# Kernel tuning notes

Measured on AMD Instinct MI355X. Metric: run time of the kernel, lower is better.

The kernel has to match this reference:

```python
import jax, jax.numpy as jnp
import numpy as np

D_MODEL = 1024
NUM_HEADS = 16
D_K = D_MODEL // NUM_HEADS
SCALE = 1.0 / np.sqrt(D_K).astype(np.float32)


def _rope_cos_sin(T, d_k):
    inv_freq = 1.0 / (10000.0 ** (jnp.arange(0, d_k, 2, dtype=jnp.float32) / d_k))
    t = jnp.arange(T, dtype=jnp.float32)
    freqs = jnp.outer(t, inv_freq)                      # [T, d_k/2]
    emb = jnp.concatenate([freqs, freqs], axis=-1)      # [T, d_k]
    return jnp.cos(emb)[None, None], jnp.sin(emb)[None, None]  # [1,1,T,d_k]


def _rotate_half(x):
    x1, x2 = x[..., : x.shape[-1] // 2], x[..., x.shape[-1] // 2 :]
    return jnp.concatenate([-x2, x1], axis=-1)


def setup_inputs() -> dict:
    key = jax.random.key(0)
    ks = jax.random.split(key, 8)
    B, T, C = 2, 2048, D_MODEL
    x = jax.random.normal(ks[0], (B, T, C), dtype=jnp.float32)
    # torch nn.Linear weights are [out, in]; forward does x @ W.T
    s = 1.0 / np.sqrt(C)
    Wq = jax.random.uniform(ks[1], (C, C), jnp.float32, -s, s)
    Wk = jax.random.uniform(ks[2], (C, C), jnp.float32, -s, s)
    Wv = jax.random.uniform(ks[3], (C, C), jnp.float32, -s, s)
    Wo = jax.random.uniform(ks[4], (C, C), jnp.float32, -s, s)
    bo = jax.random.uniform(ks[5], (C,), jnp.float32, -s, s)
    sector_bias = jnp.zeros((1, NUM_HEADS, 1, 1), dtype=jnp.float32)
    sector_weights = jax.random.uniform(ks[6], (B, T), jnp.float32, 0.5, 1.5)
    # causal mask, broadcastable to [B,H,T,T]; 0 -> masked
    mask = jnp.tril(jnp.ones((T, T), dtype=jnp.int32))[None, None]
    return {
        "x": x, "Wq": Wq, "Wk": Wk, "Wv": Wv, "Wo": Wo, "bo": bo,
        "sector_bias": sector_bias, "sector_weights": sector_weights,
        "mask": mask,
    }


def reference(x, Wq, Wk, Wv, Wo, bo, sector_bias, sector_weights, mask):
    B, T, C = x.shape
    H, dk = NUM_HEADS, D_K
    q = (x @ Wq.T).reshape(B, T, H, dk).transpose(0, 2, 1, 3)  # [B,H,T,dk]
    k = (x @ Wk.T).reshape(B, T, H, dk).transpose(0, 2, 1, 3)
    v = (x @ Wv.T).reshape(B, T, H, dk).transpose(0, 2, 1, 3)
    cos, sin = _rope_cos_sin(T, dk)
    q = q * cos + _rotate_half(q) * sin
    k = k * cos + _rotate_half(k) * sin
    scores = jnp.einsum("bhqd,bhkd->bhqk", q, k) * SCALE
    scores = scores + sector_bias
    scores = scores * sector_weights[:, None, None, :]  # broadcast over key dim
    scores = jnp.where(mask == 0, -jnp.inf, scores)
    attn = jax.nn.softmax(scores, axis=-1)
    out = jnp.einsum("bhqk,bhkd->bhqd", attn, v)
    out = out.transpose(0, 2, 1, 3).reshape(B, T, C)
    return out @ Wo.T + bo
```

## Files before the change

### kernel.cpp

```cpp
#include <hip/hip_runtime.h>


typedef __bf16 bf16x8 __attribute__((ext_vector_type(8)));
typedef float f32x4 __attribute__((ext_vector_type(4)));
typedef float f32x16 __attribute__((ext_vector_type(16)));
typedef unsigned short u16x8 __attribute__((ext_vector_type(8)));

__device__ __forceinline__ unsigned short f2bf(float f) {
    union { float f; unsigned int u; } c; c.f = f;
    unsigned int u = c.u;
    unsigned int r = u + 0x7fffu + ((u >> 16) & 1u);
    return (unsigned short)(r >> 16);
}
__device__ __forceinline__ unsigned cvtpk(float lo, float hi) {
    unsigned r;
    asm("v_cvt_pk_bf16_f32 %0, %1, %2" : "=v"(r) : "v"(lo), "v"(hi));
    return r;
}
__device__ __forceinline__ void plswap(unsigned a, unsigned b, unsigned& r0, unsigned& r1) {
#if __has_builtin(__builtin_amdgcn_permlane32_swap)
    auto s = __builtin_amdgcn_permlane32_swap(a, b, false, false);
    r0 = (unsigned)s[0]; r1 = (unsigned)s[1];
#else
    const int hh = (int)(threadIdx.x & 63) >> 5;
    const unsigned oa = (unsigned)__shfl_xor((int)a, 32);
    const unsigned ob = (unsigned)__shfl_xor((int)b, 32);
    r0 = hh ? ob : a;
    r1 = hh ? b : oa;
#endif
}
__device__ __forceinline__ void stage8_f32(unsigned short* dst, const float* src) {
    const float4 a = *(const float4*)src;
    const float4 b = *(const float4*)(src + 4);
    u16x8 v;
    v[0] = f2bf(a.x); v[1] = f2bf(a.y); v[2] = f2bf(a.z); v[3] = f2bf(a.w);
    v[4] = f2bf(b.x); v[5] = f2bf(b.y); v[6] = f2bf(b.z); v[7] = f2bf(b.w);
    *(u16x8*)dst = v;
}
__device__ __forceinline__ void async16(const unsigned short* g, unsigned short* l) {
    __builtin_amdgcn_global_load_lds(
        (const __attribute__((address_space(1))) void*)g,
        (__attribute__((address_space(3))) void*)l, 16, 0, 0);
}

__global__ __launch_bounds__(256) void cvt_all(
    const float* __restrict__ x, const float* __restrict__ Wq, const float* __restrict__ Wk,
    const float* __restrict__ Wv, const float* __restrict__ Wo,
    unsigned short* __restrict__ dst, int hasX, int n8)
{
    const int i = blockIdx.x * 256 + threadIdx.x;
    if (i >= n8) return;
    int r = i;
    const float* src; int off;
    const int xg = hasX ? 524288 : 0;
    if (r < xg) { src = x; off = r; }
    else {
        r -= xg;
        const int w = r >> 17, o = r & 131071;
        src = (w == 0) ? Wq : (w == 1) ? Wk : (w == 2) ? Wv : Wo;
        off = o;
    }
    stage8_f32(&dst[(size_t)i * 8], &src[(size_t)off * 8]);
}

template<int A_BF16>
__global__ __launch_bounds__(512) void gemm_qkv(
    const void* __restrict__ Av, const unsigned short* __restrict__ Wb,
    unsigned short* __restrict__ outv, const float* __restrict__ swg)
{
    constexpr int K = 1024, BK = 32, NS = K / BK;
    __shared__ __align__(16) unsigned short As[3][128 * BK];
    __shared__ __align__(16) unsigned short Bs[3][128 * BK];
    const int tid = threadIdx.x;
    const int wid = tid >> 6, lane = tid & 63, g = lane >> 4, l = lane & 15;
    const int wm = (wid & 3) * 32, wn = (wid >> 2) * 64;

    const int lin = blockIdx.x + (blockIdx.y << 3) + (blockIdx.z << 8);
    const int wg  = (lin & 7) * 96 + (lin >> 3);
    const int bx = wg & 7, by = (wg >> 3) & 31, bz = wg >> 8;
    const int m0 = by * 128, n0 = bx * 128;
    const int z = bz;
    const unsigned short* W = Wb + (size_t)z * 1048576;

    f32x4 acc[2][4];
#pragma unroll
    for (int i = 0; i < 2; ++i)
#pragma unroll
        for (int j = 0; j < 4; ++j) acc[i][j] = f32x4{0.f, 0.f, 0.f, 0.f};

    const int r  = tid >> 2;
    const int cs = (((tid & 3) ^ ((tid >> 3) & 3)) * 8);
    const int xg = (g ^ ((l >> 1) & 3)) * 8;

    auto compute = [&](int buf) {
        const unsigned short* Asr = As[buf];
        const unsigned short* Bsr = Bs[buf];
        bf16x8 af[2], bfr[4];
#pragma unroll
        for (int im = 0; im < 2; ++im) af[im]  = *(const bf16x8*)&Asr[(wm + im * 16 + l) * BK + xg];
#pragma unroll
        for (int in = 0; in < 4; ++in) bfr[in] = *(const bf16x8*)&Bsr[(wn + in * 16 + l) * BK + xg];
#pragma unroll
        for (int im = 0; im < 2; ++im)
#pragma unroll
            for (int in = 0; in < 4; ++in)
                acc[im][in] = __builtin_amdgcn_mfma_f32_16x16x32_bf16(af[im], bfr[in], acc[im][in], 0, 0, 0);
    };

    if (A_BF16) {
        const unsigned short* A = (const unsigned short*)Av;
        auto stage = [&](int buf, int k0) {
            async16(&A[(size_t)(m0 + r) * K + k0 + cs], &As[buf][wid * 512]);
            async16(&W[(size_t)(n0 + r) * K + k0 + cs], &Bs[buf][wid * 512]);
        };
        stage(0, 0);
        stage(1, BK);
        for (int ks = 0; ks < NS; ++ks) {
            if (ks + 1 < NS) asm volatile("s_waitcnt vmcnt(2)" ::: "memory");
            else             asm volatile("s_waitcnt vmcnt(0)" ::: "memory");
            __builtin_amdgcn_s_barrier();
            compute(ks % 3);
            if (ks + 2 < NS) stage((ks + 2) % 3, (ks + 2) * BK);
        }
    } else {
        auto stageF = [&](int buf, int k0) {
            const float* A = (const float*)Av;
            stage8_f32(&As[buf][r * BK + cs], &A[(size_t)(m0 + r) * K + k0 + cs]);
            async16(&W[(size_t)(n0 + r) * K + k0 + cs], &Bs[buf][wid * 512]);
        };
        stageF(0, 0);
        __syncthreads();
        for (int k0 = 0; k0 < K; k0 += BK) {
            const int cur = (k0 >> 5) & 1;
            if (k0 + BK < K) stageF(cur ^ 1, k0 + BK);
            compute(cur);
            __syncthreads();
        }
    }

    unsigned short* outq = outv + (size_t)z * 4194304;
    if (z < 2) {
        const int hq = (n0 + wn) >> 6;
        float freq[2];
#pragma unroll
        for (int in = 0; in < 2; ++in)
            freq[in] = exp2f(-(float)(in * 16 + l) * 0.41524101186f);
#pragma unroll
        for (int im = 0; im < 2; ++im)
#pragma unroll
            for (int i = 0; i < 4; ++i) {
                const int m = m0 + wm + im * 16 + g * 4 + i;
                const int b = m >> 11, t = m & 2047;
                float fw = 1.0f;
                if (z == 1) fw = 0.18033688011f * swg[(b << 11) + t];
                const size_t fq = (size_t)((b << 4) + hq) * 131072
                                + (size_t)((t >> 5) << 2) * 512
                                + (size_t)((((l >> 3) & 1) << 5) + (t & 31)) * 8 + (l & 7);
#pragma unroll
                for (int in = 0; in < 2; ++in) {
                    const float ang = (float)t * freq[in];
                    const float cs2 = __cosf(ang), sn = __sinf(ang);
                    const float x1 = acc[im][in][i], x2 = acc[im][in + 2][i];
                    outq[fq + (size_t)in * 512]       = f2bf((x1 * cs2 - x2 * sn) * fw);
                    outq[fq + (size_t)(in + 2) * 512] = f2bf((x2 * cs2 + x1 * sn) * fw);
                }
            }
    } else {
#pragma unroll
        for (int im = 0; im < 2; ++im)
#pragma unroll
            for (int in = 0; in < 4; ++in) {
                const int n = n0 + wn + in * 16 + l;
                const int h = n >> 6, d = n & 63;
                const int mb = m0 + wm + im * 16 + g * 4;
                const int bq = mb >> 11, t0 = mb & 2047;
                ushort4 pk;
                pk.x = f2bf(acc[im][in][0]); pk.y = f2bf(acc[im][in][1]);
                pk.z = f2bf(acc[im][in][2]); pk.w = f2bf(acc[im][in][3]);
                const size_t fv = (size_t)((bq << 4) + h) * 131072
                                + (size_t)(((t0 >> 5) << 2) + ((d >> 5) << 1) + ((t0 >> 4) & 1)) * 512
                                + (size_t)((((t0 >> 3) & 1) << 5) + (d & 31)) * 8 + (t0 & 7);
                *(ushort4*)&outq[fv] = pk;
            }
    }
}

__global__ __launch_bounds__(512) void gemm_proj(
    const unsigned short* __restrict__ A, const unsigned short* __restrict__ W,
    float* __restrict__ out, const float* __restrict__ bias)
{
    constexpr int K = 1024, BK = 32, NS = K / BK;
    __shared__ __align__(16) unsigned short As[3][64 * BK];
    __shared__ __align__(16) unsigned short Bs[3][128 * BK];
    const int tid = threadIdx.x;
    const int wid = tid >> 6, lane = tid & 63, g = lane >> 4, l = lane & 15;
    const int wm = (wid & 1) * 32, wn = (wid >> 1) * 32;

    const int lin = blockIdx.x + (blockIdx.y << 3);
    const int wg  = (lin & 7) * 64 + (lin >> 3);
    const int m0 = (wg >> 3) * 64, n0 = (wg & 7) * 128;

    f32x4 acc[2][2];
#pragma unroll
    for (int i = 0; i < 2; ++i)
#pragma unroll
        for (int j = 0; j < 2; ++j) acc[i][j] = f32x4{0.f, 0.f, 0.f, 0.f};

    const int r  = tid >> 2;
    const int cs = (((tid & 3) ^ ((tid >> 3) & 3)) * 8);
    const int xg = (g ^ ((l >> 1) & 3)) * 8;

    auto stage = [&](int buf, int k0) {
        if (tid < 256) async16(&A[(size_t)(m0 + r) * K + k0 + cs], &As[buf][wid * 512]);
        async16(&W[(size_t)(n0 + r) * K + k0 + cs], &Bs[buf][wid * 512]);
    };
    auto compute = [&](int buf) {
        const unsigned short* Asr = As[buf];
        const unsigned short* Bsr = Bs[buf];
        bf16x8 af[2], bfr[2];
#pragma unroll
        for (int im = 0; im < 2; ++im) af[im]  = *(const bf16x8*)&Asr[(wm + im * 16 + l) * BK + xg];
#pragma unroll
        for (int in = 0; in < 2; ++in) bfr[in] = *(const bf16x8*)&Bsr[(wn + in * 16 + l) * BK + xg];
#pragma unroll
        for (int im = 0; im < 2; ++im)
#pragma unroll
            for (int in = 0; in < 2; ++in)
                acc[im][in] = __builtin_amdgcn_mfma_f32_16x16x32_bf16(af[im], bfr[in], acc[im][in], 0, 0, 0);
    };

    stage(0, 0);
    stage(1, BK);
    for (int ks = 0; ks < NS; ++ks) {
        if (ks + 1 < NS) {
            if (wid < 4) asm volatile("s_waitcnt vmcnt(2)" ::: "memory");
            else         asm volatile("s_waitcnt vmcnt(1)" ::: "memory");
        } else {
            asm volatile("s_waitcnt vmcnt(0)" ::: "memory");
        }
        __builtin_amdgcn_s_barrier();
        compute(ks % 3);
        if (ks + 2 < NS) stage((ks + 2) % 3, (ks + 2) * BK);
    }

#pragma unroll
    for (int im = 0; im < 2; ++im)
#pragma unroll
        for (int in = 0; in < 2; ++in) {
            const int n = n0 + wn + in * 16 + l;
#pragma unroll
            for (int i = 0; i < 4; ++i) {
                const int m = m0 + wm + im * 16 + g * 4 + i;
                out[(size_t)m * 1024 + n] = acc[im][in][i] + bias[n];
            }
        }
}

__global__ __launch_bounds__(128, 2) void flash_attn(
    const unsigned short* __restrict__ Qf, const unsigned short* __restrict__ Kf,
    const unsigned short* __restrict__ Vf, const float* __restrict__ sbias,
    const float* __restrict__ sw, unsigned short* __restrict__ attn)
{
    constexpr int T = 2048;
    __shared__ float Cmb[3072];

    const int tid = threadIdx.x, wid = tid >> 6, lane = tid & 63;
    const int hl = lane & 31, hh = lane >> 5;
    const int id = blockIdx.x;
    const int p  = 63 - (id >> 5);
    const int bh = id & 31, b = bh >> 4, h = bh & 15;
    const size_t fb = (size_t)bh * 131072;
    const float bias = sbias[h];
    const float* swb = sw + b * T;

    bf16x8 onef;
#pragma unroll
    for (int j = 0; j < 8; ++j) onef[j] = (__bf16)1.0f;

    const int q0 = p * 32;
    bf16x8 qf[4];
#pragma unroll
    for (int ks = 0; ks < 4; ++ks)
        qf[ks] = *(const bf16x8*)&Qf[fb + (size_t)(p * 4 + ks) * 512 + lane * 8];

    f32x16 oacc[2], lrow;
#pragma unroll
    for (int r = 0; r < 16; ++r) { oacc[0][r] = 0.f; oacc[1][r] = 0.f; lrow[r] = 0.f; }

    bf16x8 kcur[4];
    if (wid <= p) {
        const unsigned short* kb = &Kf[fb + (size_t)wid * 2048 + lane * 8];
#pragma unroll
        for (int ks = 0; ks < 4; ++ks) kcur[ks] = *(const bf16x8*)&kb[ks * 512];
    }

    for (int c = wid; c <= p; c += 2) {
        f32x16 sx;
#pragma unroll
        for (int r = 0; r < 16; ++r) sx[r] = 0.f;
        sx = __builtin_amdgcn_mfma_f32_32x32x16_bf16(kcur[0], qf[0], sx, 0, 0, 0);
        sx = __builtin_amdgcn_mfma_f32_32x32x16_bf16(kcur[1], qf[1], sx, 0, 0, 0);
        sx = __builtin_amdgcn_mfma_f32_32x32x16_bf16(kcur[2], qf[2], sx, 0, 0, 0);
        sx = __builtin_amdgcn_mfma_f32_32x32x16_bf16(kcur[3], qf[3], sx, 0, 0, 0);

        if (c + 2 <= p) {
            const unsigned short* kb = &Kf[fb + (size_t)(c + 2) * 2048 + lane * 8];
#pragma unroll
            for (int ks = 0; ks < 4; ++ks) kcur[ks] = *(const bf16x8*)&kb[ks * 512];
        }

        const unsigned short* vb = &Vf[fb + (size_t)c * 2048 + lane * 8];
        const bf16x8 vf00 = *(const bf16x8*)&vb[0];
        const bf16x8 vf01 = *(const bf16x8*)&vb[512];
        const bf16x8 vf10 = *(const bf16x8*)&vb[1024];
        const bf16x8 vf11 = *(const bf16x8*)&vb[1536];

        if (bias != 0.0f) {
            const float bn = bias * 1.44269504f;
#pragma unroll
            for (int r = 0; r < 16; ++r) {
                const int kl = (r & 3) + 8 * (r >> 2) + 4 * hh;
                sx[r] += bn * swb[c * 32 + kl];
            }
        }
        if (c == p) {
#pragma unroll
            for (int r = 0; r < 16; ++r) {
                const int kl = (r & 3) + 8 * (r >> 2) + 4 * hh;
                sx[r] = (kl <= hl) ? sx[r] : -1e30f;
            }
        }
#pragma unroll
        for (int r = 0; r < 16; ++r) sx[r] = exp2f(sx[r]);

        unsigned wds[8];
#pragma unroll
        for (int g2 = 0; g2 < 4; ++g2) {
            wds[g2 * 2]     = cvtpk(sx[g2 * 4],     sx[g2 * 4 + 1]);
            wds[g2 * 2 + 1] = cvtpk(sx[g2 * 4 + 2], sx[g2 * 4 + 3]);
        }
        bf16x8 pf[2];
#pragma unroll
        for (int ks = 0; ks < 2; ++ks) {
            unsigned a0, a1, b0, b1;
            plswap(wds[4 * ks],     wds[4 * ks + 2], a0, a1);
            plswap(wds[4 * ks + 1], wds[4 * ks + 3], b0, b1);
            union { unsigned u[4]; bf16x8 v; } pk_;
            pk_.u[0] = a0; pk_.u[1] = b0;
            pk_.u[2] = a1; pk_.u[3] = b1;
            pf[ks] = pk_.v;
        }

        lrow = __builtin_amdgcn_mfma_f32_32x32x16_bf16(pf[0], onef, lrow, 0, 0, 0);
        lrow = __builtin_amdgcn_mfma_f32_32x32x16_bf16(pf[1], onef, lrow, 0, 0, 0);

        oacc[0] = __builtin_amdgcn_mfma_f32_32x32x16_bf16(pf[0], vf00, oacc[0], 0, 0, 0);
        oacc[0] = __builtin_amdgcn_mfma_f32_32x32x16_bf16(pf[1], vf01, oacc[0], 0, 0, 0);
        oacc[1] = __builtin_amdgcn_mfma_f32_32x32x16_bf16(pf[0], vf10, oacc[1], 0, 0, 0);
        oacc[1] = __builtin_amdgcn_mfma_f32_32x32x16_bf16(pf[1], vf11, oacc[1], 0, 0, 0);
    }

    __syncthreads();
    if (wid == 1) {
#pragma unroll
        for (int dt = 0; dt < 2; ++dt)
#pragma unroll
            for (int r = 0; r < 16; ++r) Cmb[(dt * 16 + r) * 64 + lane] = oacc[dt][r];
#pragma unroll
        for (int r = 0; r < 16; ++r) Cmb[2048 + r * 64 + lane] = lrow[r];
    }
    __syncthreads();
    if (wid == 0) {
#pragma unroll
        for (int r = 0; r < 16; ++r) {
            const float li = 1.0f / (lrow[r] + Cmb[2048 + r * 64 + lane]);
            const int row = (r & 3) + 8 * (r >> 2) + 4 * hh;
            const int qr = q0 + row;
#pragma unroll
            for (int dt = 0; dt < 2; ++dt) {
                const float ov = oacc[dt][r] + Cmb[(dt * 16 + r) * 64 + lane];
                attn[(size_t)(b * T + qr) * 1024 + h * 64 + dt * 32 + hl] = f2bf(ov * li);
            }
        }
    }
}

extern "C" void kernel_launch(void* const* d_in, const int* in_sizes, int n_in,
                              void* d_out, int out_size, void* d_ws, size_t ws_size,
                              hipStream_t stream) {
    const float* x  = (const float*)d_in[0];
    const float* Wq = (const float*)d_in[1];
    const float* Wk = (const float*)d_in[2];
    const float* Wv = (const float*)d_in[3];
    const float* Wo = (const float*)d_in[4];
    const float* bo = (const float*)d_in[5];
    const float* sb = (const float*)d_in[6];
    const float* sw = (const float*)d_in[7];

    const size_t QKV_SZ = 4194304;
    const size_t W_SZ   = 1048576;
    unsigned short* ws16 = (unsigned short*)d_ws;
    const bool big = ws_size >= 2 * (4 * QKV_SZ + 4 * W_SZ);

    if (big) {
        unsigned short* xb    = ws16;
        unsigned short* Wb3   = xb + QKV_SZ;
        unsigned short* Wob   = Wb3 + 3 * W_SZ;
        unsigned short* qkv   = Wob + W_SZ;
        unsigned short* attnb = xb;

        cvt_all<<<4096, 256, 0, stream>>>(x, Wq, Wk, Wv, Wo, xb, 1, 1048576);
        gemm_qkv<1><<<dim3(8, 32, 3), 512, 0, stream>>>(xb, Wb3, qkv, sw);
        flash_attn<<<2048, 128, 0, stream>>>(qkv, qkv + QKV_SZ, qkv + 2 * QKV_SZ,
                                             sb, sw, attnb);
        gemm_proj<<<dim3(8, 64), 512, 0, stream>>>(attnb, Wob, (float*)d_out, bo);
    } else {
        unsigned short* qkv   = ws16;
        unsigned short* attnb = qkv + 3 * QKV_SZ;
        unsigned short* Wb3   = attnb;
        unsigned short* Wob   = qkv;

        cvt_all<<<1536, 256, 0, stream>>>(x, Wq, Wk, Wv, Wo, Wb3, 0, 393216);
        gemm_qkv<0><<<dim3(8, 32, 3), 512, 0, stream>>>(x, Wb3, qkv, sw);
        flash_attn<<<2048, 128, 0, stream>>>(qkv, qkv + QKV_SZ, qkv + 2 * QKV_SZ,
                                             sb, sw, attnb);
        cvt_all<<<512, 256, 0, stream>>>(x, Wo, Wo, Wo, Wo, Wob, 0, 131072);
        gemm_proj<<<dim3(8, 64), 512, 0, stream>>>(attnb, Wob, (float*)d_out, bo);
    }
}
```

Measured before the change: 181.9 us.

## Pre-tile x into MFMA fragment layout and load A directly to registers

The conversion kernel now writes x in bf16 using a tiled layout that matches the MFMA A-fragment order. The QKV GEMM can then read A fragments straight from global memory into registers, with one step of register double-buffering, and skips staging A through LDS. Only the weight tile stays in LDS, now as a 4-deep ring with a fully unrolled k-loop. This cuts LDS traffic and reduces LDS footprint, which may raise occupancy. The cost is that A is no longer shared through LDS, so more global and L2 traffic is exposed, and A latency is hidden only one step ahead.

```diff
diff --git a/kernel.cpp b/kernel.cpp
--- a/kernel.cpp
+++ b/kernel.cpp
@@ -51,16 +51,18 @@
     const int i = blockIdx.x * 256 + threadIdx.x;
     if (i >= n8) return;
     int r = i;
-    const float* src; int off;
+    const float* src; size_t soff;
     const int xg = hasX ? 524288 : 0;
-    if (r < xg) { src = x; off = r; }
-    else {
+    if (r < xg) {
+        const int lane16 = r & 15, sub = (r >> 4) & 3, kb = (r >> 6) & 31, rb = r >> 11;
+        src = x; soff = (size_t)(rb * 16 + lane16) * 128 + kb * 4 + sub;
+    } else {
         r -= xg;
         const int w = r >> 17, o = r & 131071;
         src = (w == 0) ? Wq : (w == 1) ? Wk : (w == 2) ? Wv : Wo;
-        off = o;
-    }
-    stage8_f32(&dst[(size_t)i * 8], &src[(size_t)off * 8]);
+        soff = o;
+    }
+    stage8_f32(&dst[(size_t)i * 8], &src[soff * 8]);
 }
 
 template<int A_BF16>
@@ -68,9 +70,8 @@
     const void* __restrict__ Av, const unsigned short* __restrict__ Wb,
     unsigned short* __restrict__ outv, const float* __restrict__ swg)
 {
-    constexpr int K = 1024, BK = 32, NS = K / BK;
-    __shared__ __align__(16) unsigned short As[3][128 * BK];
-    __shared__ __align__(16) unsigned short Bs[3][128 * BK];
+    constexpr int K = 1024, BK = 32;
+    __shared__ __align__(16) unsigned short Bs[4][128 * BK];
     const int tid = threadIdx.x;
     const int wid = tid >> 6, lane = tid & 63, g = lane >> 4, l = lane & 15;
     const int wm = (wid & 3) * 32, wn = (wid >> 2) * 64;
@@ -92,40 +93,56 @@
     const int cs = (((tid & 3) ^ ((tid >> 3) & 3)) * 8);
     const int xg = (g ^ ((l >> 1) & 3)) * 8;
 
-    auto compute = [&](int buf) {
-        const unsigned short* Asr = As[buf];
-        const unsigned short* Bsr = Bs[buf];
-        bf16x8 af[2], bfr[4];
-#pragma unroll
-        for (int im = 0; im < 2; ++im) af[im]  = *(const bf16x8*)&Asr[(wm + im * 16 + l) * BK + xg];
-#pragma unroll
-        for (int in = 0; in < 4; ++in) bfr[in] = *(const bf16x8*)&Bsr[(wn + in * 16 + l) * BK + xg];
-#pragma unroll
-        for (int im = 0; im < 2; ++im)
-#pragma unroll
-            for (int in = 0; in < 4; ++in)
-                acc[im][in] = __builtin_amdgcn_mfma_f32_16x16x32_bf16(af[im], bfr[in], acc[im][in], 0, 0, 0);
-    };
-
     if (A_BF16) {
-        const unsigned short* A = (const unsigned short*)Av;
-        auto stage = [&](int buf, int k0) {
-            async16(&A[(size_t)(m0 + r) * K + k0 + cs], &As[buf][wid * 512]);
-            async16(&W[(size_t)(n0 + r) * K + k0 + cs], &Bs[buf][wid * 512]);
-        };
-        stage(0, 0);
-        stage(1, BK);
-        for (int ks = 0; ks < NS; ++ks) {
-            if (ks + 1 < NS) asm volatile("s_waitcnt vmcnt(2)" ::: "memory");
-            else             asm volatile("s_waitcnt vmcnt(0)" ::: "memory");
-            __builtin_amdgcn_s_barrier();
-            compute(ks % 3);
-            if (ks + 2 < NS) stage((ks + 2) % 3, (ks + 2) * BK);
-        }
+        const unsigned short* Ab = (const unsigned short*)Av;
+        Ab += (size_t)((m0 + wm) >> 4) * 16384 + g * 128 + l * 8;
+        const unsigned short* Ab1 = Ab + 16384;
+#define QSTAGE(buf, k0) async16(&W[(size_t)(n0 + r) * K + (k0) + cs], &Bs[buf][wid * 512])
+        QSTAGE(0, 0);
+        QSTAGE(1, BK);
+        bf16x8 afX0 = *(const bf16x8*)(Ab);
+        bf16x8 afX1 = *(const bf16x8*)(Ab1);
+        bf16x8 afY0, afY1;
+#define QSTEP(ks, buf, C0, C1, N0, N1, PRE, STG, WAITN)                                      \
+    {                                                                                        \
+        asm volatile("s_waitcnt vmcnt(" #WAITN ")" ::: "memory");                            \
+        __builtin_amdgcn_s_barrier();                                                        \
+        const unsigned short* Bsr = Bs[buf];                                                 \
+        bf16x8 b0 = *(const bf16x8*)&Bsr[(wn +  0 + l) * BK + xg];                           \
+        bf16x8 b1 = *(const bf16x8*)&Bsr[(wn + 16 + l) * BK + xg];                           \
+        bf16x8 b2 = *(const bf16x8*)&Bsr[(wn + 32 + l) * BK + xg];                           \
+        bf16x8 b3 = *(const bf16x8*)&Bsr[(wn + 48 + l) * BK + xg];                           \
+        if (PRE) { N0 = *(const bf16x8*)(Ab  + (size_t)((ks) + 1) * 512);                    \
+                   N1 = *(const bf16x8*)(Ab1 + (size_t)((ks) + 1) * 512); }                  \
+        acc[0][0] = __builtin_amdgcn_mfma_f32_16x16x32_bf16(C0, b0, acc[0][0], 0, 0, 0);     \
+        acc[0][1] = __builtin_amdgcn_mfma_f32_16x16x32_bf16(C0, b1, acc[0][1], 0, 0, 0);     \
+        acc[0][2] = __builtin_amdgcn_mfma_f32_16x16x32_bf16(C0, b2, acc[0][2], 0, 0, 0);     \
+        acc[0][3] = __builtin_amdgcn_mfma_f32_16x16x32_bf16(C0, b3, acc[0][3], 0, 0, 0);     \
+        acc[1][0] = __builtin_amdgcn_mfma_f32_16x16x32_bf16(C1, b0, acc[1][0], 0, 0, 0);     \
+        acc[1][1] = __builtin_amdgcn_mfma_f32_16x16x32_bf16(C1, b1, acc[1][1], 0, 0, 0);     \
+        acc[1][2] = __builtin_amdgcn_mfma_f32_16x16x32_bf16(C1, b2, acc[1][2], 0, 0, 0);     \
+        acc[1][3] = __builtin_amdgcn_mfma_f32_16x16x32_bf16(C1, b3, acc[1][3], 0, 0, 0);     \
+        if (STG) QSTAGE(((buf) + 2) & 3, ((ks) + 2) * BK);                                   \
+    }
+        for (int t = 0; t < 7; ++t) {
+            const int k4 = t * 4;
+            QSTEP(k4 + 0, 0, afX0, afX1, afY0, afY1, 1, 1, 3)
+            QSTEP(k4 + 1, 1, afY0, afY1, afX0, afX1, 1, 1, 3)
+            QSTEP(k4 + 2, 2, afX0, afX1, afY0, afY1, 1, 1, 3)
+            QSTEP(k4 + 3, 3, afY0, afY1, afX0, afX1, 1, 1, 3)
+        }
+        QSTEP(28, 0, afX0, afX1, afY0, afY1, 1, 1, 3)
+        QSTEP(29, 1, afY0, afY1, afX0, afX1, 1, 1, 3)
+        QSTEP(30, 2, afX0, afX1, afY0, afY1, 1, 0, 3)
+        QSTEP(31, 3, afY0, afY1, afX0, afX1, 0, 0, 0)
+#undef QSTEP
+#undef QSTAGE
     } else {
+        const int cc = (tid & 3);
+        const int sl = (cc ^ ((r >> 1) & 3)) * 8;
         auto stageF = [&](int buf, int k0) {
             const float* A = (const float*)Av;
-            stage8_f32(&As[buf][r * BK + cs], &A[(size_t)(m0 + r) * K + k0 + cs]);
+            stage8_f32(&Bs[2 + buf][r * BK + sl], &A[(size_t)(m0 + r) * K + k0 + cc * 8]);
             async16(&W[(size_t)(n0 + r) * K + k0 + cs], &Bs[buf][wid * 512]);
         };
         stageF(0, 0);
@@ -133,7 +150,16 @@
         for (int k0 = 0; k0 < K; k0 += BK) {
             const int cur = (k0 >> 5) & 1;
             if (k0 + BK < K) stageF(cur ^ 1, k0 + BK);
-            compute(cur);
+            bf16x8 af[2], bfr[4];
+#pragma unroll
+            for (int im = 0; im < 2; ++im) af[im]  = *(const bf16x8*)&Bs[2 + cur][(wm + im * 16 + l) * BK + xg];
+#pragma unroll
+            for (int in = 0; in < 4; ++in) bfr[in] = *(const bf16x8*)&Bs[cur][(wn + in * 16 + l) * BK + xg];
+#pragma unroll
+            for (int im = 0; im < 2; ++im)
+#pragma unroll
+                for (int in = 0; in < 4; ++in)
+                    acc[im][in] = __builtin_amdgcn_mfma_f32_16x16x32_bf16(af[im], bfr[in], acc[im][in], 0, 0, 0);
             __syncthreads();
         }
     }
```

Result: no change. 180.4 us, median of 2 (-0.8%).
